# Optimization experiments

Measured on AMD Instinct MI355X. Metric: run time of the kernel, lower is better.

Reference implementation:

```python
import jax, jax.numpy as jnp
import numpy as np

HIDDEN = 2048
HEADS = 16
HEAD_DIM = HIDDEN // HEADS


def setup_inputs() -> dict:
    key = jax.random.key(0)
    kx, kq, kk, kv, ko = jax.random.split(key, 5)
    s = 1.0 / np.sqrt(HIDDEN)
    return {
        "x": jax.random.normal(kx, (2, 2048, HIDDEN), dtype=jnp.float32),
        "Wq": jax.random.normal(kq, (HIDDEN, HIDDEN), dtype=jnp.float32) * s,
        "Wk": jax.random.normal(kk, (HIDDEN, HIDDEN), dtype=jnp.float32) * s,
        "Wv": jax.random.normal(kv, (HIDDEN, HIDDEN), dtype=jnp.float32) * s,
        "Wo": jax.random.normal(ko, (HIDDEN, HIDDEN), dtype=jnp.float32) * s,
    }


def reference(x, Wq, Wk, Wv, Wo):
    B, S, H = x.shape
    nh, hd = HEADS, HEAD_DIM
    # projections (nn.Linear: y = x @ W.T; here W stored as [in, out] so x @ W)
    q = (x @ Wq).reshape(B, S, nh, hd).transpose(0, 2, 1, 3)  # [B,nh,S,hd]
    k = (x @ Wk).reshape(B, S, nh, hd).transpose(0, 2, 1, 3)
    v = (x @ Wv).reshape(B, S, nh, hd).transpose(0, 2, 1, 3)
    scores = jnp.einsum("bhqd,bhkd->bhqk", q, k) / jnp.sqrt(jnp.float32(hd))
    causal = jnp.tril(jnp.ones((S, S), dtype=bool))  # keep lower triangle
    scores = jnp.where(causal, scores, jnp.finfo(scores.dtype).min)
    attn = jax.nn.softmax(scores, axis=-1)
    out = jnp.einsum("bhqk,bhkd->bhqd", attn, v)
    out = out.transpose(0, 2, 1, 3).reshape(B, S, H)
    return out @ Wo
```

## Files before the change

### kernel.cpp

```cpp
#include <hip/hip_runtime.h>
#include <stdint.h>

typedef unsigned short u16;
typedef __bf16 bf16x8 __attribute__((ext_vector_type(8)));
typedef float f32x4 __attribute__((ext_vector_type(4)));

#define B_ 2
#define S_ 2048
#define H_ 2048
#define NH_ 16
#define HD_ 128

__device__ __forceinline__ u16 f2bf(float f) {
    uint32_t u = __float_as_uint(f);
    u += 0x7fff + ((u >> 16) & 1);
    return (u16)(u >> 16);
}

__device__ __forceinline__ void gl_lds16(const u16* g, u16* l) {
    __builtin_amdgcn_global_load_lds(
        (const __attribute__((address_space(1))) void*)g,
        (__attribute__((address_space(3))) void*)l, 16, 0, 0);
}

__global__ __launch_bounds__(256) void cast_x_kernel(const float* __restrict__ x, u16* __restrict__ xb) {
    int i = (blockIdx.x * 256 + threadIdx.x) * 4;
    float4 v = *(const float4*)&x[i];
    ushort4 o;
    o.x = f2bf(v.x); o.y = f2bf(v.y); o.z = f2bf(v.z); o.w = f2bf(v.w);
    *(ushort4*)&xb[i] = o;
}

__global__ __launch_bounds__(256) void transpose_cast_kernel(
        const float* __restrict__ w0, const float* __restrict__ w1,
        const float* __restrict__ w2, const float* __restrict__ w3,
        u16* __restrict__ dqkv, u16* __restrict__ dwo) {
    int z = blockIdx.z;
    const float* src = (z == 0) ? w0 : (z == 1) ? w1 : (z == 2) ? w2 : w3;
    u16* dst = (z < 3) ? (dqkv + (size_t)z * H_ * H_) : dwo;
    __shared__ float tile[32][33];
    int n0 = blockIdx.x * 32, k0 = blockIdx.y * 32;
    int tx = threadIdx.x, ty = threadIdx.y;
#pragma unroll
    for (int i = 0; i < 4; i++)
        tile[ty + i * 8][tx] = src[(size_t)(k0 + ty + i * 8) * H_ + n0 + tx];
    __syncthreads();
#pragma unroll
    for (int i = 0; i < 4; i++)
        dst[(size_t)(n0 + ty + i * 8) * H_ + k0 + tx] = f2bf(tile[tx][ty + i * 8]);
}

__global__ __launch_bounds__(256) void vtrans_kernel(const u16* __restrict__ V, u16* __restrict__ VT) {
    __shared__ u16 t[64 * 72];
    int bh = blockIdx.z;
    int s0 = blockIdx.x * 64, d0 = blockIdx.y * 64;
    const u16* src = V + (size_t)bh * S_ * HD_;
    u16* dst = VT + (size_t)bh * S_ * HD_;
    int tid = threadIdx.x;
#pragma unroll
    for (int i = 0; i < 2; i++) {
        int p = i * 256 + tid, r = p >> 3, c = p & 7;
        *(int4*)&t[r * 72 + c * 8] = *(const int4*)&src[(size_t)(s0 + r) * HD_ + d0 + c * 8];
    }
    __syncthreads();
#pragma unroll
    for (int i = 0; i < 2; i++) {
        int p = i * 256 + tid, rd = p >> 3, c = p & 7;
        u16 tmp[8];
#pragma unroll
        for (int j = 0; j < 8; j++) tmp[j] = t[(c * 8 + j) * 72 + rd];
        *(int4*)&dst[(size_t)(d0 + rd) * S_ + s0 + c * 8] = *(int4*)tmp;
    }
}

template <int MODE>
__global__ __launch_bounds__(256, 2) void gemm_bt(
        const u16* __restrict__ A, const u16* __restrict__ Bt, float* __restrict__ Cout,
        u16* __restrict__ q, u16* __restrict__ k, u16* __restrict__ v,
        int M, int N, int K) {
    __shared__ u16 As[128 * 64];
    __shared__ u16 Bs[128 * 64];
    int tid = threadIdx.x;
    int w = tid >> 6, lane = tid & 63, quad = lane >> 4, l16 = lane & 15;
    int wm = w >> 1, wn = w & 1;
    int m0 = blockIdx.y * 128, n0 = blockIdx.x * 128;

    f32x4 acc[4][4];
#pragma unroll
    for (int mi = 0; mi < 4; mi++)
#pragma unroll
        for (int ni = 0; ni < 4; ni++)
            acc[mi][ni] = (f32x4){0.f, 0.f, 0.f, 0.f};

    for (int k0 = 0; k0 < K; k0 += 64) {
        const u16* ga = A + (size_t)m0 * K + k0;
        const u16* gb = Bt + (size_t)n0 * K + k0;
#pragma unroll
        for (int j = 0; j < 4; j++) {
            int base = (j * 4 + w) * 64;
            int p = base + lane;
            int row = p >> 3;
            int c = (p & 7) ^ (row & 7);
            gl_lds16(&ga[(size_t)row * K + c * 8], &As[base * 8]);
            gl_lds16(&gb[(size_t)row * K + c * 8], &Bs[base * 8]);
        }
        __syncthreads();
#pragma unroll
        for (int ks = 0; ks < 2; ks++) {
            bf16x8 af[4], bf[4];
#pragma unroll
            for (int mi = 0; mi < 4; mi++) {
                int row = wm * 64 + mi * 16 + l16;
                af[mi] = *(const bf16x8*)&As[row * 64 + (((ks * 4 + quad) ^ (row & 7)) * 8)];
            }
#pragma unroll
            for (int ni = 0; ni < 4; ni++) {
                int row = wn * 64 + ni * 16 + l16;
                bf[ni] = *(const bf16x8*)&Bs[row * 64 + (((ks * 4 + quad) ^ (row & 7)) * 8)];
            }
#pragma unroll
            for (int mi = 0; mi < 4; mi++)
#pragma unroll
                for (int ni = 0; ni < 4; ni++)
                    acc[mi][ni] = __builtin_amdgcn_mfma_f32_16x16x32_bf16(af[mi], bf[ni], acc[mi][ni], 0, 0, 0);
        }
        __syncthreads();
    }

#pragma unroll
    for (int mi = 0; mi < 4; mi++) {
#pragma unroll
        for (int ni = 0; ni < 4; ni++) {
            int ng = n0 + wn * 64 + ni * 16 + l16;
#pragma unroll
            for (int r = 0; r < 4; r++) {
                int mg = m0 + wm * 64 + mi * 16 + quad * 4 + r;
                float val = acc[mi][ni][r];
                if (MODE == 0) {
                    int which = ng >> 11;
                    int rem = ng & 2047;
                    int h = rem >> 7, d = rem & 127;
                    int b = mg >> 11, s = mg & 2047;
                    u16* base = (which == 0) ? q : (which == 1) ? k : v;
                    base[((size_t)((b * NH_ + h) * S_ + s)) * HD_ + d] = f2bf(val);
                } else {
                    Cout[(size_t)mg * N + ng] = val;
                }
            }
        }
    }
}

__global__ __launch_bounds__(256, 2) void flash_kernel(
        const u16* __restrict__ Q, const u16* __restrict__ Kb,
        const u16* __restrict__ VT, u16* __restrict__ Ctx) {
    __shared__ u16 Ks[2][64 * 128];
    __shared__ u16 Vs[128 * 64];
    __shared__ u16 Ps[64 * 64];
    int tid = threadIdx.x;
    int w = tid >> 6, lane = tid & 63, quad = lane >> 4, l16 = lane & 15;

    int id = blockIdx.x;
    int bh = id & 31;
    int b = bh >> 4, h = bh & 15;
    int pair = id >> 5;
    int qts = pair, qtl = 31 - pair;
    int n0 = qts + 1;

    size_t bhoff = ((size_t)b * NH_ + h) * S_ * HD_;
    const u16* Qp = Q + bhoff;
    const u16* Kp = Kb + bhoff;
    const u16* Vp = VT + bhoff;

    auto stageK = [&](int t, int buf) {
        int kv0 = ((t >= n0) ? (t - n0) : t) * 64;
#pragma unroll
        for (int j = 0; j < 4; j++) {
            int base = (j * 4 + w) * 64;
            int p = base + lane;
            int row = p >> 4;
            int c = (p & 15) ^ (row & 15);
            gl_lds16(&Kp[(size_t)(kv0 + row) * HD_ + c * 8], &Ks[buf][base * 8]);
        }
    };
    auto stageV = [&](int t) {
        int kv0 = ((t >= n0) ? (t - n0) : t) * 64;
#pragma unroll
        for (int j = 0; j < 4; j++) {
            int base = (j * 4 + w) * 64;
            int p = base + lane;
            int row = p >> 3;
            int c = (p & 7) ^ (row & 7);
            gl_lds16(&Vp[(size_t)row * S_ + kv0 + c * 8], &Vs[base * 8]);
        }
    };

    int q0 = qts * 64, qw = q0 + w * 16;
    bf16x8 qf[4];
#pragma unroll
    for (int ks = 0; ks < 4; ks++)
        qf[ks] = *(const bf16x8*)&Qp[(size_t)(qw + l16) * HD_ + ks * 32 + quad * 8];

    float l_part[4] = {0.f, 0.f, 0.f, 0.f};
    f32x4 ao[8];
#pragma unroll
    for (int dt = 0; dt < 8; dt++) ao[dt] = (f32x4){0.f, 0.f, 0.f, 0.f};

    const float sl2 = 0.08838834764831845f * 1.4426950408889634f;

    auto epilogue = [&]() {
#pragma unroll
        for (int r = 0; r < 4; r++) {
            float l = l_part[r];
            l += __shfl_xor(l, 1);
            l += __shfl_xor(l, 2);
            l += __shfl_xor(l, 4);
            l += __shfl_xor(l, 8);
            float inv = 1.0f / l;
            int qg = qw + quad * 4 + r;
            size_t rowbase = ((size_t)b * S_ + qg) * H_ + h * HD_;
#pragma unroll
            for (int dt = 0; dt < 8; dt++)
                Ctx[rowbase + dt * 16 + l16] = f2bf(ao[dt][r] * inv);
        }
    };

    stageK(0, 0);

    for (int t = 0; t < 33; t++) {
        __syncthreads();
        if (t + 1 < 33) stageK(t + 1, (t + 1) & 1);
        stageV(t);
        if (t == n0) {
            epilogue();
            q0 = qtl * 64; qw = q0 + w * 16;
#pragma unroll
            for (int ks = 0; ks < 4; ks++)
                qf[ks] = *(const bf16x8*)&Qp[(size_t)(qw + l16) * HD_ + ks * 32 + quad * 8];
#pragma unroll
            for (int r = 0; r < 4; r++) l_part[r] = 0.f;
#pragma unroll
            for (int dt = 0; dt < 8; dt++) ao[dt] = (f32x4){0.f, 0.f, 0.f, 0.f};
        }
        int kv0 = ((t >= n0) ? (t - n0) : t) * 64;
        bool diag = (kv0 == q0);
        int buf = t & 1;

        f32x4 sc[4];
#pragma unroll
        for (int nt = 0; nt < 4; nt++) {
            sc[nt] = (f32x4){0.f, 0.f, 0.f, 0.f};
            int row = nt * 16 + l16;
#pragma unroll
            for (int ks = 0; ks < 4; ks++) {
                bf16x8 kf = *(const bf16x8*)&Ks[buf][row * 128 + (((ks * 4 + quad) ^ (row & 15)) * 8)];
                sc[nt] = __builtin_amdgcn_mfma_f32_16x16x32_bf16(qf[ks], kf, sc[nt], 0, 0, 0);
            }
        }

#pragma unroll
        for (int r = 0; r < 4; r++) {
            int prow = w * 16 + quad * 4 + r;
            int qg = qw + quad * 4 + r;
            float psum = 0.f;
#pragma unroll
            for (int nt = 0; nt < 4; nt++) {
                float p = exp2f(sc[nt][r] * sl2);
                if (diag && (kv0 + nt * 16 + l16 > qg)) p = 0.f;
                sc[nt][r] = p;
                psum += p;
            }
            l_part[r] += psum;
#pragma unroll
            for (int nt = 0; nt < 4; nt++) {
                int col = nt * 16 + l16;
                Ps[prow * 64 + (((col >> 3) ^ (prow & 7)) * 8) + (col & 7)] = f2bf(sc[nt][r]);
            }
        }

        __syncthreads();

#pragma unroll
        for (int kstep = 0; kstep < 2; kstep++) {
            int prow = w * 16 + l16;
            bf16x8 pf = *(const bf16x8*)&Ps[prow * 64 + (((kstep * 4 + quad) ^ (prow & 7)) * 8)];
#pragma unroll
            for (int dt = 0; dt < 8; dt++) {
                int d = dt * 16 + l16;
                bf16x8 vf = *(const bf16x8*)&Vs[d * 64 + (((kstep * 4 + quad) ^ (d & 7)) * 8)];
                ao[dt] = __builtin_amdgcn_mfma_f32_16x16x32_bf16(pf, vf, ao[dt], 0, 0, 0);
            }
        }
    }
    epilogue();
}

extern "C" void kernel_launch(void* const* d_in, const int* in_sizes, int n_in,
                              void* d_out, int out_size, void* d_ws, size_t ws_size,
                              hipStream_t stream) {
    const float* x  = (const float*)d_in[0];
    const float* Wq = (const float*)d_in[1];
    const float* Wk = (const float*)d_in[2];
    const float* Wv = (const float*)d_in[3];
    const float* Wo = (const float*)d_in[4];
    float* out = (float*)d_out;

    const size_t MB = 1024 * 1024;
    char* ws = (char*)d_ws;
    u16* Xb    = (u16*)(ws);
    u16* WqkvT = (u16*)(ws + 16 * MB);
    u16* WoT   = (u16*)(ws + 40 * MB);
    u16* Qb    = (u16*)(ws + 48 * MB);
    u16* Kbuf  = (u16*)(ws + 64 * MB);
    u16* Vbuf  = (u16*)(ws + 80 * MB);
    u16* Ctx   = (u16*)(ws + 96 * MB);
    u16* VT    = Xb;

    cast_x_kernel<<<8192, 256, 0, stream>>>(x, Xb);
    transpose_cast_kernel<<<dim3(64, 64, 4), dim3(32, 8), 0, stream>>>(Wq, Wk, Wv, Wo, WqkvT, WoT);
    gemm_bt<0><<<dim3(48, 32), 256, 0, stream>>>(Xb, WqkvT, nullptr, Qb, Kbuf, Vbuf, 4096, 6144, 2048);
    vtrans_kernel<<<dim3(32, 2, 32), 256, 0, stream>>>(Vbuf, VT);
    flash_kernel<<<512, 256, 0, stream>>>(Qb, Kbuf, VT, Ctx);
    gemm_bt<1><<<dim3(16, 32), 256, 0, stream>>>(Ctx, WoT, out, nullptr, nullptr, nullptr, 4096, 2048, 2048);
}
```

Before: 343.9 us.

## Fuse V transpose into QKV GEMM epilogue and restructure flash attention

The QKV GEMM now writes V already transposed through an LDS-staged, vectorized epilogue, which removes the separate vtrans kernel. The softmax scale is folded into Q at projection time. The flash kernel drops LDS staging of P: it computes S^T so the probabilities stay in registers, packs them with perm, and feeds them to 16x16x16 MFMAs. It launches one block per query tile (1024 blocks, occupancy hint raised to 3) instead of pairing short and long tiles. This trades the paired load balancing for less LDS traffic, fewer barriers and one fewer launch.

```diff
diff --git a/kernel.cpp b/kernel.cpp
--- a/kernel.cpp
+++ b/kernel.cpp
@@ -3,6 +3,7 @@
 
 typedef unsigned short u16;
 typedef __bf16 bf16x8 __attribute__((ext_vector_type(8)));
+typedef short s4 __attribute__((ext_vector_type(4)));
 typedef float f32x4 __attribute__((ext_vector_type(4)));
 
 #define B_ 2
@@ -11,17 +12,25 @@
 #define NH_ 16
 #define HD_ 128
 
+#define SL2f (0.08838834764831845f * 1.4426950408889634f)
+
 __device__ __forceinline__ u16 f2bf(float f) {
     uint32_t u = __float_as_uint(f);
     u += 0x7fff + ((u >> 16) & 1);
     return (u16)(u >> 16);
 }
 
+__device__ __forceinline__ uint32_t pk_bf16(float lo, float hi) {
+    return __builtin_amdgcn_perm(__float_as_uint(hi), __float_as_uint(lo), 0x07060302u);
+}
+
 __device__ __forceinline__ void gl_lds16(const u16* g, u16* l) {
     __builtin_amdgcn_global_load_lds(
         (const __attribute__((address_space(1))) void*)g,
         (__attribute__((address_space(3))) void*)l, 16, 0, 0);
 }
+
+union U2S4 { uint2 u; s4 s; };
 
 __global__ __launch_bounds__(256) void cast_x_kernel(const float* __restrict__ x, u16* __restrict__ xb) {
     int i = (blockIdx.x * 256 + threadIdx.x) * 4;
@@ -50,36 +59,14 @@
         dst[(size_t)(n0 + ty + i * 8) * H_ + k0 + tx] = f2bf(tile[tx][ty + i * 8]);
 }
 
-__global__ __launch_bounds__(256) void vtrans_kernel(const u16* __restrict__ V, u16* __restrict__ VT) {
-    __shared__ u16 t[64 * 72];
-    int bh = blockIdx.z;
-    int s0 = blockIdx.x * 64, d0 = blockIdx.y * 64;
-    const u16* src = V + (size_t)bh * S_ * HD_;
-    u16* dst = VT + (size_t)bh * S_ * HD_;
-    int tid = threadIdx.x;
-#pragma unroll
-    for (int i = 0; i < 2; i++) {
-        int p = i * 256 + tid, r = p >> 3, c = p & 7;
-        *(int4*)&t[r * 72 + c * 8] = *(const int4*)&src[(size_t)(s0 + r) * HD_ + d0 + c * 8];
-    }
-    __syncthreads();
-#pragma unroll
-    for (int i = 0; i < 2; i++) {
-        int p = i * 256 + tid, rd = p >> 3, c = p & 7;
-        u16 tmp[8];
-#pragma unroll
-        for (int j = 0; j < 8; j++) tmp[j] = t[(c * 8 + j) * 72 + rd];
-        *(int4*)&dst[(size_t)(d0 + rd) * S_ + s0 + c * 8] = *(int4*)tmp;
-    }
-}
-
 template <int MODE>
 __global__ __launch_bounds__(256, 2) void gemm_bt(
         const u16* __restrict__ A, const u16* __restrict__ Bt, float* __restrict__ Cout,
         u16* __restrict__ q, u16* __restrict__ k, u16* __restrict__ v,
         int M, int N, int K) {
-    __shared__ u16 As[128 * 64];
-    __shared__ u16 Bs[128 * 64];
+    __shared__ u16 sm[2 * 128 * 64];
+    u16* As = sm;
+    u16* Bs = sm + 128 * 64;
     int tid = threadIdx.x;
     int w = tid >> 6, lane = tid & 63, quad = lane >> 4, l16 = lane & 15;
     int wm = w >> 1, wn = w & 1;
@@ -127,45 +114,71 @@
         __syncthreads();
     }
 
-#pragma unroll
-    for (int mi = 0; mi < 4; mi++) {
-#pragma unroll
-        for (int ni = 0; ni < 4; ni++) {
-            int ng = n0 + wn * 64 + ni * 16 + l16;
-#pragma unroll
-            for (int r = 0; r < 4; r++) {
-                int mg = m0 + wm * 64 + mi * 16 + quad * 4 + r;
-                float val = acc[mi][ni][r];
-                if (MODE == 0) {
-                    int which = ng >> 11;
-                    int rem = ng & 2047;
-                    int h = rem >> 7, d = rem & 127;
-                    int b = mg >> 11, s = mg & 2047;
-                    u16* base = (which == 0) ? q : (which == 1) ? k : v;
-                    base[((size_t)((b * NH_ + h) * S_ + s)) * HD_ + d] = f2bf(val);
-                } else {
-                    Cout[(size_t)mg * N + ng] = val;
+    if (MODE == 0 && n0 >= 4096) {
+#pragma unroll
+        for (int mi = 0; mi < 4; mi++) {
+#pragma unroll
+            for (int ni = 0; ni < 4; ni++) {
+                int nl = wn * 64 + ni * 16 + l16;
+#pragma unroll
+                for (int r = 0; r < 4; r++) {
+                    int ml = wm * 64 + mi * 16 + quad * 4 + r;
+                    sm[nl * 128 + (((ml >> 3) ^ (nl & 15)) * 8) + (ml & 7)] = f2bf(acc[mi][ni][r]);
                 }
             }
         }
+        __syncthreads();
+        int b = m0 >> 11, s0 = m0 & 2047;
+#pragma unroll
+        for (int i = 0; i < 8; i++) {
+            int cu = tid + i * 256;
+            int nl = cu >> 4, mc = cu & 15;
+            int4 val = *(const int4*)&sm[nl * 128 + ((mc ^ (nl & 15)) * 8)];
+            int ngl = (n0 - 4096) + nl;
+            int h = ngl >> 7, d = ngl & 127;
+            *(int4*)&v[((size_t)((b * NH_ + h) * HD_ + d)) * S_ + s0 + mc * 8] = val;
+        }
+    } else {
+#pragma unroll
+        for (int mi = 0; mi < 4; mi++) {
+#pragma unroll
+            for (int ni = 0; ni < 4; ni++) {
+                int ng = n0 + wn * 64 + ni * 16 + l16;
+#pragma unroll
+                for (int r = 0; r < 4; r++) {
+                    int mg = m0 + wm * 64 + mi * 16 + quad * 4 + r;
+                    float val = acc[mi][ni][r];
+                    if (MODE == 0) {
+                        int which = ng >> 11;
+                        int rem = ng & 2047;
+                        int h = rem >> 7, d = rem & 127;
+                        int b = mg >> 11, s = mg & 2047;
+                        if (which == 0)
+                            q[((size_t)((b * NH_ + h) * S_ + s)) * HD_ + d] = f2bf(val * SL2f);
+                        else
+                            k[((size_t)((b * NH_ + h) * S_ + s)) * HD_ + d] = f2bf(val);
+                    } else {
+                        Cout[(size_t)mg * N + ng] = val;
+                    }
+                }
+            }
+        }
     }
 }
 
-__global__ __launch_bounds__(256, 2) void flash_kernel(
+__global__ __launch_bounds__(256, 3) void flash_kernel(
         const u16* __restrict__ Q, const u16* __restrict__ Kb,
         const u16* __restrict__ VT, u16* __restrict__ Ctx) {
     __shared__ u16 Ks[2][64 * 128];
     __shared__ u16 Vs[128 * 64];
-    __shared__ u16 Ps[64 * 64];
     int tid = threadIdx.x;
     int w = tid >> 6, lane = tid & 63, quad = lane >> 4, l16 = lane & 15;
 
     int id = blockIdx.x;
     int bh = id & 31;
     int b = bh >> 4, h = bh & 15;
-    int pair = id >> 5;
-    int qts = pair, qtl = 31 - pair;
-    int n0 = qts + 1;
+    int qt = 31 - (id >> 5);
+    int q0 = qt * 64;
 
     size_t bhoff = ((size_t)b * NH_ + h) * S_ * HD_;
     const u16* Qp = Q + bhoff;
@@ -173,7 +186,7 @@
     const u16* Vp = VT + bhoff;
 
     auto stageK = [&](int t, int buf) {
-        int kv0 = ((t >= n0) ? (t - n0) : t) * 64;
+        int kv0 = t * 64;
 #pragma unroll
         for (int j = 0; j < 4; j++) {
             int base = (j * 4 + w) * 64;
@@ -184,7 +197,7 @@
         }
     };
     auto stageV = [&](int t) {
-        int kv0 = ((t >= n0) ? (t - n0) : t) * 64;
+        int kv0 = t * 64;
 #pragma unroll
         for (int j = 0; j < 4; j++) {
             int base = (j * 4 + w) * 64;
@@ -195,56 +208,25 @@
         }
     };
 
-    int q0 = qts * 64, qw = q0 + w * 16;
+    int qw = q0 + w * 16;
+    int qg = qw + l16;
     bf16x8 qf[4];
 #pragma unroll
     for (int ks = 0; ks < 4; ks++)
-        qf[ks] = *(const bf16x8*)&Qp[(size_t)(qw + l16) * HD_ + ks * 32 + quad * 8];
-
-    float l_part[4] = {0.f, 0.f, 0.f, 0.f};
+        qf[ks] = *(const bf16x8*)&Qp[(size_t)qg * HD_ + ks * 32 + quad * 8];
+
+    float l_part = 0.f;
     f32x4 ao[8];
 #pragma unroll
     for (int dt = 0; dt < 8; dt++) ao[dt] = (f32x4){0.f, 0.f, 0.f, 0.f};
 
-    const float sl2 = 0.08838834764831845f * 1.4426950408889634f;
-
-    auto epilogue = [&]() {
-#pragma unroll
-        for (int r = 0; r < 4; r++) {
-            float l = l_part[r];
-            l += __shfl_xor(l, 1);
-            l += __shfl_xor(l, 2);
-            l += __shfl_xor(l, 4);
-            l += __shfl_xor(l, 8);
-            float inv = 1.0f / l;
-            int qg = qw + quad * 4 + r;
-            size_t rowbase = ((size_t)b * S_ + qg) * H_ + h * HD_;
-#pragma unroll
-            for (int dt = 0; dt < 8; dt++)
-                Ctx[rowbase + dt * 16 + l16] = f2bf(ao[dt][r] * inv);
-        }
-    };
-
     stageK(0, 0);
 
-    for (int t = 0; t < 33; t++) {
-        __syncthreads();
-        if (t + 1 < 33) stageK(t + 1, (t + 1) & 1);
+    for (int t = 0; t <= qt; t++) {
+        int buf = t & 1;
+        __syncthreads();
+        if (t < qt) stageK(t + 1, (t + 1) & 1);
         stageV(t);
-        if (t == n0) {
-            epilogue();
-            q0 = qtl * 64; qw = q0 + w * 16;
-#pragma unroll
-            for (int ks = 0; ks < 4; ks++)
-                qf[ks] = *(const bf16x8*)&Qp[(size_t)(qw + l16) * HD_ + ks * 32 + quad * 8];
-#pragma unroll
-            for (int r = 0; r < 4; r++) l_part[r] = 0.f;
-#pragma unroll
-            for (int dt = 0; dt < 8; dt++) ao[dt] = (f32x4){0.f, 0.f, 0.f, 0.f};
-        }
-        int kv0 = ((t >= n0) ? (t - n0) : t) * 64;
-        bool diag = (kv0 == q0);
-        int buf = t & 1;
 
         f32x4 sc[4];
 #pragma unroll
@@ -254,45 +236,63 @@
 #pragma unroll
             for (int ks = 0; ks < 4; ks++) {
                 bf16x8 kf = *(const bf16x8*)&Ks[buf][row * 128 + (((ks * 4 + quad) ^ (row & 15)) * 8)];
-                sc[nt] = __builtin_amdgcn_mfma_f32_16x16x32_bf16(qf[ks], kf, sc[nt], 0, 0, 0);
-            }
-        }
-
-#pragma unroll
-        for (int r = 0; r < 4; r++) {
-            int prow = w * 16 + quad * 4 + r;
-            int qg = qw + quad * 4 + r;
-            float psum = 0.f;
+                sc[nt] = __builtin_amdgcn_mfma_f32_16x16x32_bf16(kf, qf[ks], sc[nt], 0, 0, 0);
+            }
+        }
+
+        U2S4 pk[4];
+        if (t < qt) {
 #pragma unroll
             for (int nt = 0; nt < 4; nt++) {
-                float p = exp2f(sc[nt][r] * sl2);
-                if (diag && (kv0 + nt * 16 + l16 > qg)) p = 0.f;
-                sc[nt][r] = p;
-                psum += p;
-            }
-            l_part[r] += psum;
+                float p0 = exp2f(sc[nt][0]), p1 = exp2f(sc[nt][1]);
+                float p2 = exp2f(sc[nt][2]), p3 = exp2f(sc[nt][3]);
+                l_part += (p0 + p1) + (p2 + p3);
+                pk[nt].u.x = pk_bf16(p0, p1);
+                pk[nt].u.y = pk_bf16(p2, p3);
+            }
+        } else {
+            int kvb = t * 64 + quad * 4;
 #pragma unroll
             for (int nt = 0; nt < 4; nt++) {
-                int col = nt * 16 + l16;
-                Ps[prow * 64 + (((col >> 3) ^ (prow & 7)) * 8) + (col & 7)] = f2bf(sc[nt][r]);
-            }
-        }
-
-        __syncthreads();
-
-#pragma unroll
-        for (int kstep = 0; kstep < 2; kstep++) {
-            int prow = w * 16 + l16;
-            bf16x8 pf = *(const bf16x8*)&Ps[prow * 64 + (((kstep * 4 + quad) ^ (prow & 7)) * 8)];
+                int kv = kvb + nt * 16;
+                float p0 = (kv + 0 > qg) ? 0.f : exp2f(sc[nt][0]);
+                float p1 = (kv + 1 > qg) ? 0.f : exp2f(sc[nt][1]);
+                float p2 = (kv + 2 > qg) ? 0.f : exp2f(sc[nt][2]);
+                float p3 = (kv + 3 > qg) ? 0.f : exp2f(sc[nt][3]);
+                l_part += (p0 + p1) + (p2 + p3);
+                pk[nt].u.x = pk_bf16(p0, p1);
+                pk[nt].u.y = pk_bf16(p2, p3);
+            }
+        }
+
+        __syncthreads();
+
+#pragma unroll
+        for (int kt = 0; kt < 4; kt++) {
 #pragma unroll
             for (int dt = 0; dt < 8; dt++) {
                 int d = dt * 16 + l16;
-                bf16x8 vf = *(const bf16x8*)&Vs[d * 64 + (((kstep * 4 + quad) ^ (d & 7)) * 8)];
-                ao[dt] = __builtin_amdgcn_mfma_f32_16x16x32_bf16(pf, vf, ao[dt], 0, 0, 0);
+                int c = kt * 2 + (quad >> 1);
+                s4 va = *(const s4*)&Vs[d * 64 + ((c ^ (d & 7)) * 8) + (quad & 1) * 4];
+                ao[dt] = __builtin_amdgcn_mfma_f32_16x16x16bf16_1k(va, pk[kt].s, ao[dt], 0, 0, 0);
             }
         }
     }
-    epilogue();
+
+    float l = l_part;
+    l += __shfl_xor(l, 16);
+    l += __shfl_xor(l, 32);
+    float inv = 1.0f / l;
+    size_t base = ((size_t)b * S_ + qg) * H_ + h * HD_;
+#pragma unroll
+    for (int dt = 0; dt < 8; dt++) {
+        float a0 = ao[dt][0] * inv, a1 = ao[dt][1] * inv;
+        float a2 = ao[dt][2] * inv, a3 = ao[dt][3] * inv;
+        uint2 st;
+        st.x = pk_bf16(a0, a1);
+        st.y = pk_bf16(a2, a3);
+        *(uint2*)&Ctx[base + dt * 16 + quad * 4] = st;
+    }
 }
 
 extern "C" void kernel_launch(void* const* d_in, const int* in_sizes, int n_in,
@@ -312,14 +312,12 @@
     u16* WoT   = (u16*)(ws + 40 * MB);
     u16* Qb    = (u16*)(ws + 48 * MB);
     u16* Kbuf  = (u16*)(ws + 64 * MB);
-    u16* Vbuf  = (u16*)(ws + 80 * MB);
+    u16* VT    = (u16*)(ws + 80 * MB);
     u16* Ctx   = (u16*)(ws + 96 * MB);
-    u16* VT    = Xb;
 
     cast_x_kernel<<<8192, 256, 0, stream>>>(x, Xb);
     transpose_cast_kernel<<<dim3(64, 64, 4), dim3(32, 8), 0, stream>>>(Wq, Wk, Wv, Wo, WqkvT, WoT);
-    gemm_bt<0><<<dim3(48, 32), 256, 0, stream>>>(Xb, WqkvT, nullptr, Qb, Kbuf, Vbuf, 4096, 6144, 2048);
-    vtrans_kernel<<<dim3(32, 2, 32), 256, 0, stream>>>(Vbuf, VT);
-    flash_kernel<<<512, 256, 0, stream>>>(Qb, Kbuf, VT, Ctx);
+    gemm_bt<0><<<dim3(48, 32), 256, 0, stream>>>(Xb, WqkvT, nullptr, Qb, Kbuf, VT, 4096, 6144, 2048);
+    flash_kernel<<<1024, 256, 0, stream>>>(Qb, Kbuf, VT, Ctx);
     gemm_bt<1><<<dim3(16, 32), 256, 0, stream>>>(Ctx, WoT, out, nullptr, nullptr, nullptr, 4096, 2048, 2048);
 }
```

New measurement: 354.2 us. 1.03x slower.
